# Kernel optimization log

Hardware: AMD Instinct MI355X
Metric: run time of the kernel (lower is better)

The kernel has to match this reference:

```python
import jax, jax.numpy as jnp
import numpy as np

K = 10  # num_s nearest neighbors


def setup_inputs() -> dict:
    key = jax.random.key(0)
    k1, k2, k3, k4 = jax.random.split(key, 4)
    B, N, D, DO = 128, 50000, 384, 2048
    return {
        "targets": jax.random.normal(k1, (B, D), dtype=jnp.float32),
        "data": jax.random.normal(k2, (N, D), dtype=jnp.float32),
        "OTinput": jax.random.normal(k3, (N, D), dtype=jnp.float32),
        "OToutput": jax.random.normal(k4, (N, DO), dtype=jnp.float32),
    }


def reference(targets, data, OTinput, OToutput):
    # torch.cdist (p=2): sqrt(||t||^2 + ||d||^2 - 2 t.d), computed via one GEMM
    t2 = jnp.sum(targets * targets, axis=1, keepdims=True)        # [B, 1]
    d2 = jnp.sum(data * data, axis=1)[None, :]                    # [1, N]
    sq = t2 + d2 - 2.0 * jnp.einsum('bd,nd->bn', targets, data)  # [B, N]
    dist = jnp.sqrt(jnp.maximum(sq, 0.0))
    # topk smallest -> top_k of negated distances
    _, indices = jax.lax.top_k(-dist, K)                          # [B, K]
    input_local = OTinput[indices]                                # [B, K, D]
    output_local = OToutput[indices]                              # [B, K, DO]
    return input_local, output_local
```

## Files before the change

kernel.cpp:

```cpp
#include <hip/hip_runtime.h>
#include <hip/hip_bf16.h>

#define DIM   384
#define DIMO  2048
#define KNN   10
#define KSEL  16
#define FINF  3.0e38f
#define BK    64
#define PITCH 72

typedef __attribute__((ext_vector_type(8))) short short8v;
typedef __attribute__((ext_vector_type(4))) float float4v;

__device__ __forceinline__ unsigned short f2bf(float x) {
    return __bfloat16_as_ushort(__float2bfloat16(x));
}

__global__ __launch_bounds__(256) void score_topk_kernel(
    const float* __restrict__ tgt,
    const float* __restrict__ dat,
    float* __restrict__ cand_s,
    int*   __restrict__ cand_i,
    int N, int nblk)
{
    __shared__ unsigned short tAB[2 * 128 * PITCH];
    unsigned short* tA = tAB;
    unsigned short* tB = tAB + 128 * PITCH;
    float (*sc)[129] = reinterpret_cast<float(*)[129]>(tAB);
    __shared__ float d2p[128][8];
    __shared__ float d2s[128];

    const int tid   = threadIdx.x;
    const int nbase = blockIdx.x * 128;
    const int lane  = tid & 63;
    const int wv    = tid >> 6;
    const int wr    = wv >> 1;
    const int wc    = wv & 1;
    const int r0    = tid >> 3;
    const int c8    = tid & 7;

    const int frow  = lane & 15;
    const int kg    = lane >> 4;

    float4v acc[4][4];
#pragma unroll
    for (int i = 0; i < 4; ++i)
#pragma unroll
        for (int j = 0; j < 4; ++j) acc[i][j] = (float4v){0.f, 0.f, 0.f, 0.f};

    float d2acc[4] = {0.f, 0.f, 0.f, 0.f};

    for (int k0 = 0; k0 < DIM; k0 += BK) {
        __syncthreads();
#pragma unroll
        for (int it = 0; it < 4; ++it) {
            int row = it * 32 + r0;
            const float* s = &tgt[row * DIM + k0 + c8 * 8];
            float4 u0 = *reinterpret_cast<const float4*>(s);
            float4 u1 = *reinterpret_cast<const float4*>(s + 4);
            short8v h;
            h[0] = (short)f2bf(u0.x); h[1] = (short)f2bf(u0.y);
            h[2] = (short)f2bf(u0.z); h[3] = (short)f2bf(u0.w);
            h[4] = (short)f2bf(u1.x); h[5] = (short)f2bf(u1.y);
            h[6] = (short)f2bf(u1.z); h[7] = (short)f2bf(u1.w);
            *reinterpret_cast<short8v*>(&tA[row * PITCH + c8 * 8]) = h;
        }
#pragma unroll
        for (int it = 0; it < 4; ++it) {
            int row = it * 32 + r0;
            int g   = nbase + row;
            float4 u0 = make_float4(0.f, 0.f, 0.f, 0.f);
            float4 u1 = make_float4(0.f, 0.f, 0.f, 0.f);
            if (g < N) {
                const float* s = &dat[(size_t)g * DIM + k0 + c8 * 8];
                u0 = *reinterpret_cast<const float4*>(s);
                u1 = *reinterpret_cast<const float4*>(s + 4);
            }
            d2acc[it] += u0.x * u0.x + u0.y * u0.y + u0.z * u0.z + u0.w * u0.w
                       + u1.x * u1.x + u1.y * u1.y + u1.z * u1.z + u1.w * u1.w;
            short8v h;
            h[0] = (short)f2bf(u0.x); h[1] = (short)f2bf(u0.y);
            h[2] = (short)f2bf(u0.z); h[3] = (short)f2bf(u0.w);
            h[4] = (short)f2bf(u1.x); h[5] = (short)f2bf(u1.y);
            h[6] = (short)f2bf(u1.z); h[7] = (short)f2bf(u1.w);
            *reinterpret_cast<short8v*>(&tB[row * PITCH + c8 * 8]) = h;
        }
        __syncthreads();
#pragma unroll
        for (int ks = 0; ks < 2; ++ks) {
            short8v a[4], b[4];
            const int koff = ks * 32 + kg * 8;
#pragma unroll
            for (int f = 0; f < 4; ++f) {
                a[f] = *reinterpret_cast<const short8v*>(
                    &tA[(wr * 64 + f * 16 + frow) * PITCH + koff]);
                b[f] = *reinterpret_cast<const short8v*>(
                    &tB[(wc * 64 + f * 16 + frow) * PITCH + koff]);
            }
#pragma unroll
            for (int fr = 0; fr < 4; ++fr)
#pragma unroll
                for (int fc = 0; fc < 4; ++fc)
                    acc[fr][fc] = __builtin_amdgcn_mfma_f32_16x16x32_bf16(
                        a[fr], b[fc], acc[fr][fc], 0, 0, 0);
        }
    }

    __syncthreads();
#pragma unroll
    for (int it = 0; it < 4; ++it) d2p[it * 32 + r0][c8] = d2acc[it];
    __syncthreads();
    if (tid < 128) {
        float s = 0.f;
#pragma unroll
        for (int j = 0; j < 8; ++j) s += d2p[tid][j];
        d2s[tid] = s;
    }

    const int M = nblk * KNN;
    for (int h = 0; h < 2; ++h) {
        __syncthreads();
        if (wr == h) {
#pragma unroll
            for (int fr = 0; fr < 4; ++fr)
#pragma unroll
                for (int fc = 0; fc < 4; ++fc)
#pragma unroll
                    for (int e = 0; e < 4; ++e) {
                        int lr = fr * 16 + kg * 4 + e;
                        int lc = wc * 64 + fc * 16 + frow;
                        int n  = nbase + lc;
                        sc[lr][lc] = (n < N) ? d2s[lc] - 2.f * acc[fr][fc][e]
                                             : FINF;
                    }
        }
        __syncthreads();
        if (tid < 64) {
            int grow = h * 64 + tid;
            float ts[KNN];
            int   ti[KNN];
#pragma unroll
            for (int k = 0; k < KNN; ++k) { ts[k] = FINF; ti[k] = 0x7fffffff; }
            for (int c = 0; c < 128; ++c) {
                float s = sc[tid][c];
                if (s < ts[KNN - 1]) {
                    ts[KNN - 1] = s;
                    ti[KNN - 1] = nbase + c;
#pragma unroll
                    for (int p = KNN - 1; p > 0; --p) {
                        if (ts[p] < ts[p - 1]) {
                            float fs = ts[p]; ts[p] = ts[p - 1]; ts[p - 1] = fs;
                            int   fi = ti[p]; ti[p] = ti[p - 1]; ti[p - 1] = fi;
                        }
                    }
                }
            }
            size_t base = (size_t)grow * M + (size_t)blockIdx.x * KNN;
#pragma unroll
            for (int k = 0; k < KNN; ++k) {
                cand_s[base + k] = ts[k];
                cand_i[base + k] = ti[k];
            }
        }
    }
}

__global__ __launch_bounds__(256) void select_rescore_gather_kernel(
    const float* __restrict__ cand_s,
    const int*   __restrict__ cand_i,
    const float* __restrict__ tgt,
    const float* __restrict__ dat,
    const float* __restrict__ OTin,
    const float* __restrict__ OTout,
    float* __restrict__ out,
    int M, int B)
{
    const int b    = blockIdx.x;
    const int tid  = threadIdx.x;
    const int lane = tid & 63;
    const int wv   = tid >> 6;
    const float* rs_ = cand_s + (size_t)b * M;
    const int*   ri_ = cand_i + (size_t)b * M;

    float ts[KSEL];
    int   ti[KSEL];
#pragma unroll
    for (int k = 0; k < KSEL; ++k) { ts[k] = FINF; ti[k] = 0x7fffffff; }

    for (int j = tid; j < M; j += 256) {
        float s  = rs_[j];
        int   id = ri_[j];
        if (s < ts[KSEL - 1] || (s == ts[KSEL - 1] && id < ti[KSEL - 1])) {
            ts[KSEL - 1] = s;
            ti[KSEL - 1] = id;
#pragma unroll
            for (int p = KSEL - 1; p > 0; --p) {
                bool sw = (ts[p] < ts[p - 1]) ||
                          (ts[p] == ts[p - 1] && ti[p] < ti[p - 1]);
                if (sw) {
                    float fs = ts[p]; ts[p] = ts[p - 1]; ts[p - 1] = fs;
                    int   fi = ti[p]; ti[p] = ti[p - 1]; ti[p - 1] = fi;
                }
            }
        }
    }

    __shared__ float ls[256 * KSEL];
    __shared__ int   li[256 * KSEL];
    __shared__ float wout_s[4 * KSEL];
    __shared__ int   wout_i[4 * KSEL];
    __shared__ int   sel16[KSEL];
    __shared__ float ex_s[KSEL];
    __shared__ int   ex_i[KSEL];
    __shared__ int   selk[KNN];

#pragma unroll
    for (int k = 0; k < KSEL; ++k) {
        ls[tid * KSEL + k] = ts[k];
        li[tid * KSEL + k] = ti[k];
    }

    {
        int   hp = 0;
        float hs = ts[0];
        int   hi = ti[0];
#pragma unroll
        for (int k = 0; k < KSEL; ++k) {
            float ms = hs; int mi = hi;
#pragma unroll
            for (int m = 32; m > 0; m >>= 1) {
                float s2 = __shfl_xor(ms, m);
                int   i2 = __shfl_xor(mi, m);
                if (s2 < ms || (s2 == ms && i2 < mi)) { ms = s2; mi = i2; }
            }
            if (lane == 0) { wout_s[wv * KSEL + k] = ms; wout_i[wv * KSEL + k] = mi; }
            bool iwin = (hs == ms) && (hi == mi);
            if (iwin) {
                if (hp < KSEL - 1) {
                    ++hp;
                    hs = ls[tid * KSEL + hp];
                    hi = li[tid * KSEL + hp];
                } else {
                    hs = FINF; hi = 0x7fffffff;
                }
            }
        }
    }
    __syncthreads();

    if (wv == 0) {
        float s = wout_s[lane];
        int   i = wout_i[lane];
#pragma unroll
        for (int k = 0; k < KSEL; ++k) {
            float ms = s; int mi = i;
#pragma unroll
            for (int m = 32; m > 0; m >>= 1) {
                float s2 = __shfl_xor(ms, m);
                int   i2 = __shfl_xor(mi, m);
                if (s2 < ms || (s2 == ms && i2 < mi)) { ms = s2; mi = i2; }
            }
            if (lane == 0) sel16[k] = mi;
            if (s == ms && i == mi) { s = FINF; i = 0x7fffffff; }
        }
    }
    __syncthreads();

    if (tid < KSEL) {
        const int n = sel16[tid];
        float d2p_[8] = {0.f, 0.f, 0.f, 0.f, 0.f, 0.f, 0.f, 0.f};
        float dot = 0.f;
        for (int c = 0; c < DIM / 32; ++c) {
#pragma unroll
            for (int j = 0; j < 8; ++j) {
                const float4 v = *reinterpret_cast<const float4*>(
                    &dat[(size_t)n * DIM + c * 32 + j * 4]);
                const float4 t = *reinterpret_cast<const float4*>(
                    &tgt[(size_t)b * DIM + c * 32 + j * 4]);
                d2p_[j] += v.x * v.x + v.y * v.y + v.z * v.z + v.w * v.w;
                dot = fmaf(t.x, v.x, dot);
                dot = fmaf(t.y, v.y, dot);
                dot = fmaf(t.z, v.z, dot);
                dot = fmaf(t.w, v.w, dot);
            }
        }
        float d2 = 0.f;
#pragma unroll
        for (int j = 0; j < 8; ++j) d2 += d2p_[j];
        ex_s[tid] = d2 - 2.f * dot;
        ex_i[tid] = n;
    }
    __syncthreads();

    if (tid == 0) {
        float fs[KNN]; int fi[KNN];
#pragma unroll
        for (int k = 0; k < KNN; ++k) { fs[k] = FINF; fi[k] = 0x7fffffff; }
        for (int q = 0; q < KSEL; ++q) {
            float s  = ex_s[q];
            int   id = ex_i[q];
            if (s < fs[KNN - 1] || (s == fs[KNN - 1] && id < fi[KNN - 1])) {
                fs[KNN - 1] = s;
                fi[KNN - 1] = id;
#pragma unroll
                for (int p = KNN - 1; p > 0; --p) {
                    bool sw = (fs[p] < fs[p - 1]) ||
                              (fs[p] == fs[p - 1] && fi[p] < fi[p - 1]);
                    if (sw) {
                        float a = fs[p]; fs[p] = fs[p - 1]; fs[p - 1] = a;
                        int   i2 = fi[p]; fi[p] = fi[p - 1]; fi[p - 1] = i2;
                    }
                }
            }
        }
#pragma unroll
        for (int k = 0; k < KNN; ++k) selk[k] = fi[k];
    }
    __syncthreads();

    const size_t o1 = (size_t)B * KNN * DIM;
    const float4* in4  = reinterpret_cast<const float4*>(OTin);
    const float4* ino4 = reinterpret_cast<const float4*>(OTout);
    float4* out4  = reinterpret_cast<float4*>(out);
    float4* outo4 = reinterpret_cast<float4*>(out + o1);

    for (int q = tid; q < KNN * (DIM / 4); q += 256) {
        int k = q / (DIM / 4);
        int c = q - k * (DIM / 4);
        int idx = selk[k];
        out4[((size_t)b * KNN + k) * (DIM / 4) + c] =
            in4[(size_t)idx * (DIM / 4) + c];
    }
    for (int q = tid; q < KNN * (DIMO / 4); q += 256) {
        int k = q / (DIMO / 4);
        int c = q - k * (DIMO / 4);
        int idx = selk[k];
        outo4[((size_t)b * KNN + k) * (DIMO / 4) + c] =
            ino4[(size_t)idx * (DIMO / 4) + c];
    }
}

extern "C" void kernel_launch(void* const* d_in, const int* in_sizes, int n_in,
                              void* d_out, int out_size, void* d_ws, size_t ws_size,
                              hipStream_t stream) {
    const float* targets = (const float*)d_in[0];
    const float* data    = (const float*)d_in[1];
    const float* OTin    = (const float*)d_in[2];
    const float* OTout   = (const float*)d_in[3];
    float* out = (float*)d_out;

    const int B = in_sizes[0] / DIM;
    const int N = in_sizes[1] / DIM;

    const int nblk = (N + 127) / 128;
    const int M    = nblk * KNN;

    float* cand_s = (float*)d_ws;
    int*   cand_i = (int*)(cand_s + (size_t)B * M);

    score_topk_kernel<<<nblk, 256, 0, stream>>>(targets, data, cand_s, cand_i, N, nblk);
    select_rescore_gather_kernel<<<B, 256, 0, stream>>>(
        cand_s, cand_i, targets, data, OTin, OTout, out, M, B);
}
```

Measured before the change: 156.8 us.

## Split per-block top-k across two threads per row and widen gather grid

```diff
diff --git a/kernel.cpp b/kernel.cpp
--- a/kernel.cpp
+++ b/kernel.cpp
@@ -13,7 +13,9 @@
 typedef __attribute__((ext_vector_type(4))) float float4v;
 
 __device__ __forceinline__ unsigned short f2bf(float x) {
-    return __bfloat16_as_ushort(__float2bfloat16(x));
+    union { float f; unsigned u; } c; c.f = x;
+    unsigned lsb = (c.u >> 16) & 1u;
+    return (unsigned short)((c.u + 0x7FFFu + lsb) >> 16);
 }
 
 __global__ __launch_bounds__(256) void score_topk_kernel(
@@ -29,6 +31,8 @@
     float (*sc)[129] = reinterpret_cast<float(*)[129]>(tAB);
     __shared__ float d2p[128][8];
     __shared__ float d2s[128];
+    __shared__ float mgs[64][2][KNN];
+    __shared__ int   mgi[64][2][KNN];
 
     const int tid   = threadIdx.x;
     const int nbase = blockIdx.x * 128;
@@ -38,7 +42,6 @@
     const int wc    = wv & 1;
     const int r0    = tid >> 3;
     const int c8    = tid & 7;
-
     const int frow  = lane & 15;
     const int kg    = lane >> 4;
 
@@ -58,12 +61,12 @@
             const float* s = &tgt[row * DIM + k0 + c8 * 8];
             float4 u0 = *reinterpret_cast<const float4*>(s);
             float4 u1 = *reinterpret_cast<const float4*>(s + 4);
-            short8v h;
-            h[0] = (short)f2bf(u0.x); h[1] = (short)f2bf(u0.y);
-            h[2] = (short)f2bf(u0.z); h[3] = (short)f2bf(u0.w);
-            h[4] = (short)f2bf(u1.x); h[5] = (short)f2bf(u1.y);
-            h[6] = (short)f2bf(u1.z); h[7] = (short)f2bf(u1.w);
-            *reinterpret_cast<short8v*>(&tA[row * PITCH + c8 * 8]) = h;
+            short8v hh;
+            hh[0] = (short)f2bf(u0.x); hh[1] = (short)f2bf(u0.y);
+            hh[2] = (short)f2bf(u0.z); hh[3] = (short)f2bf(u0.w);
+            hh[4] = (short)f2bf(u1.x); hh[5] = (short)f2bf(u1.y);
+            hh[6] = (short)f2bf(u1.z); hh[7] = (short)f2bf(u1.w);
+            *reinterpret_cast<short8v*>(&tA[row * PITCH + c8 * 8]) = hh;
         }
 #pragma unroll
         for (int it = 0; it < 4; ++it) {
@@ -78,12 +81,12 @@
             }
             d2acc[it] += u0.x * u0.x + u0.y * u0.y + u0.z * u0.z + u0.w * u0.w
                        + u1.x * u1.x + u1.y * u1.y + u1.z * u1.z + u1.w * u1.w;
-            short8v h;
-            h[0] = (short)f2bf(u0.x); h[1] = (short)f2bf(u0.y);
-            h[2] = (short)f2bf(u0.z); h[3] = (short)f2bf(u0.w);
-            h[4] = (short)f2bf(u1.x); h[5] = (short)f2bf(u1.y);
-            h[6] = (short)f2bf(u1.z); h[7] = (short)f2bf(u1.w);
-            *reinterpret_cast<short8v*>(&tB[row * PITCH + c8 * 8]) = h;
+            short8v hh;
+            hh[0] = (short)f2bf(u0.x); hh[1] = (short)f2bf(u0.y);
+            hh[2] = (short)f2bf(u0.z); hh[3] = (short)f2bf(u0.w);
+            hh[4] = (short)f2bf(u1.x); hh[5] = (short)f2bf(u1.y);
+            hh[6] = (short)f2bf(u1.z); hh[7] = (short)f2bf(u1.w);
+            *reinterpret_cast<short8v*>(&tB[row * PITCH + c8 * 8]) = hh;
         }
         __syncthreads();
 #pragma unroll
@@ -135,37 +138,50 @@
                     }
         }
         __syncthreads();
-        if (tid < 64) {
-            int grow = h * 64 + tid;
+        if (tid < 128) {
+            int r = tid >> 1, p = tid & 1;
             float ts[KNN];
             int   ti[KNN];
 #pragma unroll
             for (int k = 0; k < KNN; ++k) { ts[k] = FINF; ti[k] = 0x7fffffff; }
-            for (int c = 0; c < 128; ++c) {
-                float s = sc[tid][c];
+            for (int c = p; c < 128; c += 2) {
+                float s = sc[r][c];
                 if (s < ts[KNN - 1]) {
                     ts[KNN - 1] = s;
                     ti[KNN - 1] = nbase + c;
 #pragma unroll
-                    for (int p = KNN - 1; p > 0; --p) {
-                        if (ts[p] < ts[p - 1]) {
-                            float fs = ts[p]; ts[p] = ts[p - 1]; ts[p - 1] = fs;
-                            int   fi = ti[p]; ti[p] = ti[p - 1]; ti[p - 1] = fi;
+                    for (int q = KNN - 1; q > 0; --q) {
+                        if (ts[q] < ts[q - 1]) {
+                            float fs = ts[q]; ts[q] = ts[q - 1]; ts[q - 1] = fs;
+                            int   fi = ti[q]; ti[q] = ti[q - 1]; ti[q - 1] = fi;
                         }
                     }
                 }
             }
-            size_t base = (size_t)grow * M + (size_t)blockIdx.x * KNN;
 #pragma unroll
             for (int k = 0; k < KNN; ++k) {
-                cand_s[base + k] = ts[k];
-                cand_i[base + k] = ti[k];
+                mgs[r][p][k] = ts[k];
+                mgi[r][p][k] = ti[k];
+            }
+        }
+        __syncthreads();
+        if (tid < 64) {
+            int r = tid;
+            int i0 = 0, i1 = 0;
+            size_t base = (size_t)(h * 64 + r) * M + (size_t)blockIdx.x * KNN;
+#pragma unroll
+            for (int k = 0; k < KNN; ++k) {
+                float s0 = mgs[r][0][i0], s1 = mgs[r][1][i1];
+                int   a0 = mgi[r][0][i0], a1 = mgi[r][1][i1];
+                bool take0 = (s0 < s1) || (s0 == s1 && a0 < a1);
+                if (take0) { cand_s[base + k] = s0; cand_i[base + k] = a0; ++i0; }
+                else       { cand_s[base + k] = s1; cand_i[base + k] = a1; ++i1; }
             }
         }
     }
 }
 
-__global__ __launch_bounds__(256) void select_rescore_gather_kernel(
+__global__ __launch_bounds__(256) void select_gather_kernel(
     const float* __restrict__ cand_s,
     const int*   __restrict__ cand_i,
     const float* __restrict__ tgt,
@@ -175,7 +191,9 @@
     float* __restrict__ out,
     int M, int B)
 {
-    const int b    = blockIdx.x;
+    const int u    = blockIdx.x;
+    const int b    = u / KNN;
+    const int kk   = u - b * KNN;
     const int tid  = threadIdx.x;
     const int lane = tid & 63;
     const int wv   = tid >> 6;
@@ -234,15 +252,12 @@
                 if (s2 < ms || (s2 == ms && i2 < mi)) { ms = s2; mi = i2; }
             }
             if (lane == 0) { wout_s[wv * KSEL + k] = ms; wout_i[wv * KSEL + k] = mi; }
-            bool iwin = (hs == ms) && (hi == mi);
-            if (iwin) {
+            if (hs == ms && hi == mi) {
                 if (hp < KSEL - 1) {
                     ++hp;
                     hs = ls[tid * KSEL + hp];
                     hi = li[tid * KSEL + hp];
-                } else {
-                    hs = FINF; hi = 0x7fffffff;
-                }
+                } else { hs = FINF; hi = 0x7fffffff; }
             }
         }
     }
@@ -318,26 +333,15 @@
     }
     __syncthreads();
 
+    const int idx = selk[kk];
     const size_t o1 = (size_t)B * KNN * DIM;
-    const float4* in4  = reinterpret_cast<const float4*>(OTin);
-    const float4* ino4 = reinterpret_cast<const float4*>(OTout);
-    float4* out4  = reinterpret_cast<float4*>(out);
-    float4* outo4 = reinterpret_cast<float4*>(out + o1);
-
-    for (int q = tid; q < KNN * (DIM / 4); q += 256) {
-        int k = q / (DIM / 4);
-        int c = q - k * (DIM / 4);
-        int idx = selk[k];
-        out4[((size_t)b * KNN + k) * (DIM / 4) + c] =
-            in4[(size_t)idx * (DIM / 4) + c];
-    }
-    for (int q = tid; q < KNN * (DIMO / 4); q += 256) {
-        int k = q / (DIMO / 4);
-        int c = q - k * (DIMO / 4);
-        int idx = selk[k];
-        outo4[((size_t)b * KNN + k) * (DIMO / 4) + c] =
-            ino4[(size_t)idx * (DIMO / 4) + c];
-    }
+    const float4* in4  = reinterpret_cast<const float4*>(&OTin[(size_t)idx * DIM]);
+    float4*       out4 = reinterpret_cast<float4*>(&out[(size_t)u * DIM]);
+    for (int q = tid; q < DIM / 4; q += 256) out4[q] = in4[q];
+
+    const float4* ino4  = reinterpret_cast<const float4*>(&OTout[(size_t)idx * DIMO]);
+    float4*       outo4 = reinterpret_cast<float4*>(&out[o1 + (size_t)u * DIMO]);
+    for (int q = tid; q < DIMO / 4; q += 256) outo4[q] = ino4[q];
 }
 
 extern "C" void kernel_launch(void* const* d_in, const int* in_sizes, int n_in,
@@ -359,6 +363,6 @@
     int*   cand_i = (int*)(cand_s + (size_t)B * M);
 
     score_topk_kernel<<<nblk, 256, 0, stream>>>(targets, data, cand_s, cand_i, N, nblk);
-    select_rescore_gather_kernel<<<B, 256, 0, stream>>>(
+    select_gather_kernel<<<B * KNN, 256, 0, stream>>>(
         cand_s, cand_i, targets, data, OTin, OTout, out, M, B);
 }
```

Result: slower. 200.3 us (+27.7%).
